# Performance work log

Measured on AMD Instinct MI355X. Metric: run time of the kernel, lower is better.

## Reference

```python
import jax, jax.numpy as jnp
import numpy as np
from jax import lax

# Module config (from init_kwargs)
PADDING = (1, 1)
DILATION = (1, 1)
GROUPS = 1
# stride param is initialized to ones(2); effective integer stride = floor(stride) = (1, 1).
# Output shape depends on this value, so it must be static under jit.
INT_STRIDE = (1, 1)


def setup_inputs() -> dict:
    key = jax.random.key(0)
    k1, k2 = jax.random.split(key)
    B, Cin, H, W = 32, 128, 64, 64
    Cout, kH, kW = 256, 3, 3
    x = jax.random.normal(k1, (B, Cin, H, W), dtype=jnp.float32)
    # reset_parameters: uniform(-stdv, stdv), stdv = 1/sqrt(Cin*kH*kW)
    stdv = 1.0 / np.sqrt(Cin * kH * kW)
    weight = jax.random.uniform(k2, (Cout, Cin // GROUPS, kH, kW), dtype=jnp.float32,
                                minval=-stdv, maxval=stdv)
    stride = jnp.ones((2,), dtype=jnp.float32)
    return {"x": x, "weight": weight, "stride": stride}


def reference(x, weight, stride):
    # Integer strides = floor(stride); with stride initialized to ones this is (1, 1).
    # (Static under jit; floor has zero derivative a.e., so stride only affects
    #  sampling locations, exactly as in the CUDA im2col forward.)
    out = lax.conv_general_dilated(
        x, weight,
        window_strides=INT_STRIDE,
        padding=[(PADDING[0], PADDING[0]), (PADDING[1], PADDING[1])],
        rhs_dilation=DILATION,
        dimension_numbers=("NCHW", "OIHW", "NCHW"),
        feature_group_count=GROUPS,
    )
    return out
```

## Files before the change

### kernel.cpp

```cpp
#include <hip/hip_runtime.h>

typedef __attribute__((ext_vector_type(8))) short short8;
typedef __attribute__((ext_vector_type(4))) float f32x4;

#define XP_ELEMS (32u * 66u * 66u * 128u)
#define WT_ELEMS (256u * 1152u)
#define WS_NEED  ((size_t)(XP_ELEMS + WT_ELEMS) * 2u)

typedef const __attribute__((address_space(1))) void* gp1_t;
typedef __attribute__((address_space(3))) void* lp3_t;

__device__ __forceinline__ void gload16(const void* g, void* l) {
  __builtin_amdgcn_global_load_lds((gp1_t)g, (lp3_t)l, 16, 0, 0);
}

__device__ __forceinline__ short f2bf(float f) {
  unsigned u = __float_as_uint(f);
  u = (u + 0x7FFFu + ((u >> 16) & 1u)) >> 16;
  return (short)u;
}

__global__ __launch_bounds__(256) void prepass_x(const float* __restrict__ x,
                                                 short* __restrict__ xp) {
  __shared__ short lds[64 * 128];
  const int y = blockIdx.x;
  const int b = blockIdx.y;
  const int t = threadIdx.x;

  const float* src = x + (long)b * 128 * 4096 + y * 64;
#pragma unroll
  for (int i = 0; i < 8; ++i) {
    int f4 = t + i * 256;
    int cin = f4 >> 4, px4 = f4 & 15;
    float4 v = *(const float4*)(src + (long)cin * 4096 + px4 * 4);
    float vv[4] = {v.x, v.y, v.z, v.w};
#pragma unroll
    for (int j = 0; j < 4; ++j) {
      int px = px4 * 4 + j;
      int g = (cin >> 3) ^ ((px ^ (px >> 2)) & 15);
      lds[px * 128 + (g << 3) + (cin & 7)] = f2bf(vv[j]);
    }
  }
  __syncthreads();
  short* dst = xp + ((long)(b * 66 + y + 1) * 66 + 1) * 128;
#pragma unroll
  for (int i = 0; i < 4; ++i) {
    int f8 = t + i * 256;
    int px = f8 >> 4, c8 = f8 & 15;
    int g = c8 ^ ((px ^ (px >> 2)) & 15);
    short8 v = *(const short8*)&lds[px * 128 + (g << 3)];
    *(short8*)(dst + (long)px * 128 + c8 * 8) = v;
  }
  short8 z = (short8)0;
  short* rowbase = xp + (long)(b * 66 + y + 1) * 66 * 128;
  if (t < 32) {
    int px = (t < 16) ? 0 : 65;
    int c8 = t & 15;
    *(short8*)(rowbase + (long)px * 128 + c8 * 8) = z;
  }
  if (y == 0) {
    short* r0 = xp + (long)(b * 66) * 66 * 128;
    for (int idx = t; idx < 66 * 16; idx += 256) *(short8*)(r0 + idx * 8) = z;
  }
  if (y == 63) {
    short* r65 = xp + ((long)(b * 66) + 65) * 66 * 128;
    for (int idx = t; idx < 66 * 16; idx += 256) *(short8*)(r65 + idx * 8) = z;
  }
}

__global__ __launch_bounds__(256) void prepass_w(const float* __restrict__ w,
                                                 short* __restrict__ wt) {
  int o    = blockIdx.x * 256 + threadIdx.x;
  int cout = o / 1152;
  int r    = o % 1152;
  int kh   = r / 384;
  int kw   = (r / 128) % 3;
  int cin  = r & 127;
  wt[o] = f2bf(w[((cout * 128 + cin) * 3 + kh) * 3 + kw]);
}

__global__ __launch_bounds__(256) void conv_gemm(const short* __restrict__ xp,
                                                 const short* __restrict__ wt,
                                                 float* __restrict__ out) {
  __shared__ short Alds[128 * 32];
  __shared__ short Blds[128 * 32];
  const int tid   = threadIdx.x;
  const int w     = tid >> 6;
  const int l     = tid & 63;
  const int l15   = l & 15;
  const int q     = l >> 4;
  const int ntile = blockIdx.x;
  const int m0    = blockIdx.y << 7;

  const int srow = (w << 4) + (l >> 2);
  const int sch8 = (((l & 3) ^ ((srow >> 1) & 3)) * 8);

  const long aoff0 = (long)(m0 + srow) * 1152 + sch8;
  const long aoff1 = aoff0 + (long)64 * 1152;

  long boff[2];
#pragma unroll
  for (int c = 0; c < 2; ++c) {
    int ng = (ntile << 7) + (c << 6) + srow;
    int b = ng >> 12, yx = ng & 4095;
    int y = yx >> 6, xx = yx & 63;
    boff[c] = ((long)(b * 66 + y) * 66 + xx) * 128 + sch8;
  }

  short* Adst0 = &Alds[(w << 4) * 32];
  short* Adst1 = Adst0 + 64 * 32;
  short* Bdst0 = &Blds[(w << 4) * 32];
  short* Bdst1 = Bdst0 + 64 * 32;

  f32x4 acc[4][4];
#pragma unroll
  for (int i = 0; i < 4; ++i)
#pragma unroll
    for (int j = 0; j < 4; ++j) acc[i][j] = (f32x4)0.f;

  const int wm = (w >> 1) << 6;
  const int wn = (w & 1) << 6;

#pragma unroll
  for (int khkw = 0; khkw < 9; ++khkw) {
    const int kh = khkw / 3, kw = khkw % 3;
    const long sB = (long)(kh * 66 + kw) * 128;
    const int kkb = khkw << 7;
#pragma unroll
    for (int c4 = 0; c4 < 4; ++c4) {
      const int cin0 = c4 << 5;
      const int kk0  = kkb + cin0;
      gload16(wt + aoff0 + kk0, Adst0);
      gload16(wt + aoff1 + kk0, Adst1);
      gload16(xp + boff[0] + sB + cin0, Bdst0);
      gload16(xp + boff[1] + sB + cin0, Bdst1);
      __syncthreads();
      short8 af[4], bf[4];
#pragma unroll
      for (int i = 0; i < 4; ++i) {
        int rA = wm + (i << 4) + l15;
        af[i] = *(const short8*)&Alds[rA * 32 + ((q ^ ((rA >> 1) & 3)) << 3)];
      }
#pragma unroll
      for (int j = 0; j < 4; ++j) {
        int rB = wn + (j << 4) + l15;
        bf[j] = *(const short8*)&Blds[rB * 32 + ((q ^ ((rB >> 1) & 3)) << 3)];
      }
#pragma unroll
      for (int i = 0; i < 4; ++i)
#pragma unroll
        for (int j = 0; j < 4; ++j)
          acc[i][j] = __builtin_amdgcn_mfma_f32_16x16x32_bf16(af[i], bf[j],
                                                              acc[i][j], 0, 0, 0);
      __syncthreads();
    }
  }

  const int ngb = (ntile << 7) + wn;
  const int b   = ngb >> 12;
  const int yxb = ngb & 4095;
  float* outb = out + (long)b * (256 * 4096) + yxb + l15;
#pragma unroll
  for (int i = 0; i < 4; ++i) {
#pragma unroll
    for (int r = 0; r < 4; ++r) {
      const int cout = m0 + wm + (i << 4) + q * 4 + r;
      float* orow = outb + (long)cout * 4096;
#pragma unroll
      for (int j = 0; j < 4; ++j) orow[j * 16] = acc[i][j][r];
    }
  }
}

__global__ __launch_bounds__(256) void naive_conv(const float* __restrict__ x,
                                                  const float* __restrict__ wgt,
                                                  float* __restrict__ out) {
  long o = (long)blockIdx.x * 256 + threadIdx.x;
  int xx = (int)(o & 63);
  int y  = (int)((o >> 6) & 63);
  int co = (int)((o >> 12) & 255);
  int b  = (int)(o >> 20);
  float s = 0.f;
  for (int ci = 0; ci < 128; ++ci) {
    for (int kh = 0; kh < 3; ++kh) {
      int iy = y + kh - 1;
      if (iy < 0 || iy > 63) continue;
      for (int kw = 0; kw < 3; ++kw) {
        int ix = xx + kw - 1;
        if (ix < 0 || ix > 63) continue;
        s += x[((long)(b * 128 + ci) * 64 + iy) * 64 + ix] *
             wgt[((co * 128 + ci) * 3 + kh) * 3 + kw];
      }
    }
  }
  out[o] = s;
}

extern "C" void kernel_launch(void* const* d_in, const int* in_sizes, int n_in,
                              void* d_out, int out_size, void* d_ws, size_t ws_size,
                              hipStream_t stream) {
  (void)in_sizes; (void)n_in;
  const float* x   = (const float*)d_in[0];
  const float* wgt = (const float*)d_in[1];
  float* out = (float*)d_out;
  if (ws_size >= WS_NEED) {
    short* xp = (short*)d_ws;
    short* wt = xp + XP_ELEMS;
    prepass_x<<<dim3(64, 32), dim3(256), 0, stream>>>(x, xp);
    prepass_w<<<dim3(WT_ELEMS / 256), dim3(256), 0, stream>>>(wgt, wt);
    conv_gemm<<<dim3(1024, 2), dim3(256), 0, stream>>>(xp, wt, out);
  } else {
    naive_conv<<<dim3(out_size / 256), dim3(256), 0, stream>>>(x, wgt, out);
  }
}
```

Before: 274.3 us.

## Halve GEMM N-tile for higher occupancy and fuse prepass kernels

The conv GEMM block tile shrinks from 128x128 to 128x64 output, each wave now computes 64x32, and launch bounds request 5 blocks per SM, with the grid doubled to match. The aim is more resident waves to hide load and barrier latency, at the cost of lower operand reuse per LDS load and twice as many weight tile fetches. The separate input and weight conversion kernels are merged into a single launch, with block index selecting the role, to save one kernel launch.

```diff
diff --git a/kernel.cpp b/kernel.cpp
--- a/kernel.cpp
+++ b/kernel.cpp
@@ -20,12 +20,24 @@
   return (short)u;
 }
 
-__global__ __launch_bounds__(256) void prepass_x(const float* __restrict__ x,
-                                                 short* __restrict__ xp) {
+__global__ __launch_bounds__(256) void prepass(const float* __restrict__ x,
+                                               const float* __restrict__ wg,
+                                               short* __restrict__ xp,
+                                               short* __restrict__ wt) {
   __shared__ short lds[64 * 128];
-  const int y = blockIdx.x;
-  const int b = blockIdx.y;
   const int t = threadIdx.x;
+  if (blockIdx.x >= 2048) {
+    int o    = (blockIdx.x - 2048) * 256 + t;
+    int cout = o / 1152;
+    int r    = o % 1152;
+    int kh   = r / 384;
+    int kw   = (r / 128) % 3;
+    int cin  = r & 127;
+    wt[o] = f2bf(wg[((cout * 128 + cin) * 3 + kh) * 3 + kw]);
+    return;
+  }
+  const int y = blockIdx.x & 63;
+  const int b = blockIdx.x >> 6;
 
   const float* src = x + (long)b * 128 * 4096 + y * 64;
 #pragma unroll
@@ -68,22 +80,11 @@
   }
 }
 
-__global__ __launch_bounds__(256) void prepass_w(const float* __restrict__ w,
-                                                 short* __restrict__ wt) {
-  int o    = blockIdx.x * 256 + threadIdx.x;
-  int cout = o / 1152;
-  int r    = o % 1152;
-  int kh   = r / 384;
-  int kw   = (r / 128) % 3;
-  int cin  = r & 127;
-  wt[o] = f2bf(w[((cout * 128 + cin) * 3 + kh) * 3 + kw]);
-}
-
-__global__ __launch_bounds__(256) void conv_gemm(const short* __restrict__ xp,
-                                                 const short* __restrict__ wt,
-                                                 float* __restrict__ out) {
+__global__ __launch_bounds__(256, 5) void conv_gemm(const short* __restrict__ xp,
+                                                    const short* __restrict__ wt,
+                                                    float* __restrict__ out) {
   __shared__ short Alds[128 * 32];
-  __shared__ short Blds[128 * 32];
+  __shared__ short Blds[64 * 32];
   const int tid   = threadIdx.x;
   const int w     = tid >> 6;
   const int l     = tid & 63;
@@ -98,28 +99,26 @@
   const long aoff0 = (long)(m0 + srow) * 1152 + sch8;
   const long aoff1 = aoff0 + (long)64 * 1152;
 
-  long boff[2];
-#pragma unroll
-  for (int c = 0; c < 2; ++c) {
-    int ng = (ntile << 7) + (c << 6) + srow;
+  long boff;
+  {
+    int ng = (ntile << 6) + srow;
     int b = ng >> 12, yx = ng & 4095;
     int y = yx >> 6, xx = yx & 63;
-    boff[c] = ((long)(b * 66 + y) * 66 + xx) * 128 + sch8;
+    boff = ((long)(b * 66 + y) * 66 + xx) * 128 + sch8;
   }
 
   short* Adst0 = &Alds[(w << 4) * 32];
   short* Adst1 = Adst0 + 64 * 32;
-  short* Bdst0 = &Blds[(w << 4) * 32];
-  short* Bdst1 = Bdst0 + 64 * 32;
-
-  f32x4 acc[4][4];
+  short* Bdst  = &Blds[(w << 4) * 32];
+
+  f32x4 acc[4][2];
 #pragma unroll
   for (int i = 0; i < 4; ++i)
 #pragma unroll
-    for (int j = 0; j < 4; ++j) acc[i][j] = (f32x4)0.f;
+    for (int j = 0; j < 2; ++j) acc[i][j] = (f32x4)0.f;
 
   const int wm = (w >> 1) << 6;
-  const int wn = (w & 1) << 6;
+  const int wn = (w & 1) << 5;
 
 #pragma unroll
   for (int khkw = 0; khkw < 9; ++khkw) {
@@ -132,31 +131,30 @@
       const int kk0  = kkb + cin0;
       gload16(wt + aoff0 + kk0, Adst0);
       gload16(wt + aoff1 + kk0, Adst1);
-      gload16(xp + boff[0] + sB + cin0, Bdst0);
-      gload16(xp + boff[1] + sB + cin0, Bdst1);
+      gload16(xp + boff + sB + cin0, Bdst);
       __syncthreads();
-      short8 af[4], bf[4];
+      short8 af[4], bf[2];
 #pragma unroll
       for (int i = 0; i < 4; ++i) {
         int rA = wm + (i << 4) + l15;
         af[i] = *(const short8*)&Alds[rA * 32 + ((q ^ ((rA >> 1) & 3)) << 3)];
       }
 #pragma unroll
-      for (int j = 0; j < 4; ++j) {
+      for (int j = 0; j < 2; ++j) {
         int rB = wn + (j << 4) + l15;
         bf[j] = *(const short8*)&Blds[rB * 32 + ((q ^ ((rB >> 1) & 3)) << 3)];
       }
 #pragma unroll
       for (int i = 0; i < 4; ++i)
 #pragma unroll
-        for (int j = 0; j < 4; ++j)
+        for (int j = 0; j < 2; ++j)
           acc[i][j] = __builtin_amdgcn_mfma_f32_16x16x32_bf16(af[i], bf[j],
                                                               acc[i][j], 0, 0, 0);
       __syncthreads();
     }
   }
 
-  const int ngb = (ntile << 7) + wn;
+  const int ngb = (ntile << 6) + wn;
   const int b   = ngb >> 12;
   const int yxb = ngb & 4095;
   float* outb = out + (long)b * (256 * 4096) + yxb + l15;
@@ -167,7 +165,7 @@
       const int cout = m0 + wm + (i << 4) + q * 4 + r;
       float* orow = outb + (long)cout * 4096;
 #pragma unroll
-      for (int j = 0; j < 4; ++j) orow[j * 16] = acc[i][j][r];
+      for (int j = 0; j < 2; ++j) orow[j * 16] = acc[i][j][r];
     }
   }
 }
@@ -206,9 +204,8 @@
   if (ws_size >= WS_NEED) {
     short* xp = (short*)d_ws;
     short* wt = xp + XP_ELEMS;
-    prepass_x<<<dim3(64, 32), dim3(256), 0, stream>>>(x, xp);
-    prepass_w<<<dim3(WT_ELEMS / 256), dim3(256), 0, stream>>>(wgt, wt);
-    conv_gemm<<<dim3(1024, 2), dim3(256), 0, stream>>>(xp, wt, out);
+    prepass<<<dim3(2048 + WT_ELEMS / 256), dim3(256), 0, stream>>>(x, wgt, xp, wt);
+    conv_gemm<<<dim3(2048, 2), dim3(256), 0, stream>>>(xp, wt, out);
   } else {
     naive_conv<<<dim3(out_size / 256), dim3(256), 0, stream>>>(x, wgt, out);
   }
```

After: 296.4 us. 1.08x slower.
